# Performance work log

Measured on AMD Instinct MI355X. Metric: run time of the kernel, lower is better.

Reference implementation:

```python
import jax, jax.numpy as jnp
import numpy as np

BN_EPS = 1e-5

def _bn_relu(x, gamma, beta):
    # x: [E, B, F]; BatchNorm1d in training mode: batch stats over B, biased var
    mu = jnp.mean(x, axis=1, keepdims=True)
    var = jnp.mean(jnp.square(x - mu), axis=1, keepdims=True)
    y = gamma[:, None, :] * (x - mu) * jax.lax.rsqrt(var + BN_EPS) + beta[:, None, :]
    return jax.nn.relu(y)

def setup_inputs() -> dict:
    key = jax.random.key(0)
    ks = jax.random.split(key, 4)
    B, D, E, H1, H2, T = 32768, 1472, 8, 512, 256, 2
    s1 = (2.0 / D) ** 0.5
    s2 = (2.0 / H1) ** 0.5
    return {
        "x_deep": jax.random.normal(ks[0], (B, D), jnp.float32),
        "W1": jax.random.normal(ks[1], (E, D, H1), jnp.float32) * s1,
        "b1": jnp.zeros((E, H1), jnp.float32),
        "g1": jnp.ones((E, H1), jnp.float32),
        "be1": jnp.zeros((E, H1), jnp.float32),
        "W2": jax.random.normal(ks[2], (E, H1, H2), jnp.float32) * s2,
        "b2": jnp.zeros((E, H2), jnp.float32),
        "g2": jnp.ones((E, H2), jnp.float32),
        "be2": jnp.zeros((E, H2), jnp.float32),
        "Wg": jax.random.normal(ks[3], (T, D, E), jnp.float32) * s1,
        "bg": jnp.zeros((T, E), jnp.float32),
    }

def reference(x_deep, W1, b1, g1, be1, W2, b2, g2, be2, Wg, bg):
    # Experts: batched over expert dim E (replaces Python loop over nn.ModuleList)
    h = jnp.einsum('bd,edh->ebh', x_deep, W1) + b1[:, None, :]   # [E,B,H1]
    h = _bn_relu(h, g1, be1)                                     # dropout: identity (eval)
    h = jnp.einsum('ebh,ehk->ebk', h, W2) + b2[:, None, :]       # [E,B,H2]
    experts_out = _bn_relu(h, g2, be2)                           # [E,B,H2]
    # Gates: [T,B,E], softmax over experts
    gates = jax.nn.softmax(jnp.einsum('bd,tde->tbe', x_deep, Wg) + bg[:, None, :], axis=-1)
    # Combine: task_out[t] = reshape(experts_out * gate[...,None], [B, E*H2])
    task = experts_out[None, :, :, :] * jnp.transpose(gates, (0, 2, 1))[:, :, :, None]  # [T,E,B,H2]
    T, E, B, H2 = task.shape
    out = jnp.transpose(task, (0, 2, 1, 3)).reshape(T, B, E * H2)  # [T,B,E*H2]
    return out
```

## Files before the change

### kernel.cpp

```cpp
#include <hip/hip_runtime.h>
#include <cstdint>


typedef __attribute__((ext_vector_type(8))) __bf16 bf16x8;
typedef __attribute__((ext_vector_type(4))) float f32x4;

__device__ __forceinline__ unsigned short f2bf(float f) {
  unsigned int u = __float_as_uint(f);
  u += 0x7fffu + ((u >> 16) & 1u);
  return (unsigned short)(u >> 16);
}
__device__ __forceinline__ float bf2f(unsigned short s) {
  return __uint_as_float(((unsigned int)s) << 16);
}

__device__ __forceinline__ void async16(const void* g, void* l) {
  __builtin_amdgcn_global_load_lds((__attribute__((address_space(1))) unsigned int*)g,
                                   (__attribute__((address_space(3))) unsigned int*)l,
                                   16, 0, 0);
}

__global__ void convert_f32_bf16(const float* __restrict__ in,
                                 unsigned short* __restrict__ out, size_t n) {
  size_t i = ((size_t)blockIdx.x * blockDim.x + threadIdx.x) * 4;
  if (i + 3 < n) {
    float4 v = *(const float4*)(in + i);
    unsigned int w0 = (unsigned int)f2bf(v.x) | ((unsigned int)f2bf(v.y) << 16);
    unsigned int w1 = (unsigned int)f2bf(v.z) | ((unsigned int)f2bf(v.w) << 16);
    *(uint2*)(out + i) = make_uint2(w0, w1);
  }
}

__global__ void transpose_bf16(const float* __restrict__ W,
                               unsigned short* __restrict__ Wt, int D, int H) {
  __shared__ float tile[32][33];
  int e = blockIdx.z;
  int d0 = blockIdx.x * 32, h0 = blockIdx.y * 32;
  const float* We = W + (size_t)e * D * H;
  unsigned short* Wte = Wt + (size_t)e * D * H;
  int tx = threadIdx.x, ty = threadIdx.y;
#pragma unroll
  for (int i = 0; i < 4; ++i)
    tile[ty + i * 8][tx] = We[(size_t)(d0 + ty + i * 8) * H + h0 + tx];
  __syncthreads();
#pragma unroll
  for (int i = 0; i < 4; ++i)
    Wte[(size_t)(h0 + ty + i * 8) * D + d0 + tx] = f2bf(tile[tx][ty + i * 8]);
}

__global__ void transpose_wg(const float* __restrict__ Wg,
                             unsigned short* __restrict__ Wt, int D) {
  int idx = blockIdx.x * 256 + threadIdx.x;
  int te = idx / D, d = idx - te * D;
  int t = te >> 3, e = te & 7;
  Wt[(size_t)te * D + d] = f2bf(Wg[((size_t)t * D + d) * 8 + e]);
}

__global__ __launch_bounds__(256) void gemm_bt(
    const unsigned short* __restrict__ A, int lda,
    const unsigned short* __restrict__ Bt,
    unsigned short* __restrict__ C, int ldc, int K,
    size_t aStrideE, size_t bStrideE, size_t cStrideE,
    float* __restrict__ sum, float* __restrict__ sq, int statStrideE, int statCols,
    int groupM, int GN) {
  __shared__ unsigned short sA[128 * 32];
  __shared__ unsigned short sB[128 * 32];
  const int tid = threadIdx.x;
  const int e = blockIdx.z;

  int bx, by;
  if (groupM) {
    int bid = blockIdx.x;
    int gsize = groupM * GN;
    int gid = bid / gsize;
    int rem = bid - gid * gsize;
    bx = gid * groupM + rem % groupM;
    by = rem / groupM;
  } else {
    bx = blockIdx.x; by = blockIdx.y;
  }

  const unsigned short* Ae = A + (size_t)e * aStrideE + (size_t)bx * 128 * lda;
  const unsigned short* Be = Bt + (size_t)e * bStrideE + (size_t)by * 128 * K;

  const int lrow = tid >> 2;
  const int lseg = (tid & 3) * 8;
  const int wid = tid >> 6, lane = tid & 63;
  const int wr = (wid & 1) * 64, wc = (wid >> 1) * 64;
  const int mrow = lane & 15;
  const int kg = (lane >> 4) * 8;

  f32x4 acc[4][4] = {};
  const unsigned short* ga = Ae + (size_t)lrow * lda + lseg;
  const unsigned short* gb = Be + (size_t)lrow * K + lseg;
  const size_t aHalf = (size_t)64 * lda;
  const size_t bHalf = (size_t)64 * K;

  for (int k0 = 0; k0 < K; k0 += 32) {
    async16(ga + k0,         &sA[tid * 8]);
    async16(ga + k0 + aHalf, &sA[2048 + tid * 8]);
    async16(gb + k0,         &sB[tid * 8]);
    async16(gb + k0 + bHalf, &sB[2048 + tid * 8]);
    __syncthreads();
    bf16x8 af[4], bfr[4];
#pragma unroll
    for (int i = 0; i < 4; ++i)
      af[i] = *(const bf16x8*)&sA[(wr + i * 16 + mrow) * 32 + kg];
#pragma unroll
    for (int j = 0; j < 4; ++j)
      bfr[j] = *(const bf16x8*)&sB[(wc + j * 16 + mrow) * 32 + kg];
#pragma unroll
    for (int i = 0; i < 4; ++i)
#pragma unroll
      for (int j = 0; j < 4; ++j)
        acc[i][j] = __builtin_amdgcn_mfma_f32_16x16x32_bf16(af[i], bfr[j], acc[i][j], 0, 0, 0);
    __syncthreads();
  }

  unsigned short* Ce = C + (size_t)e * cStrideE + (size_t)bx * 128 * ldc +
                       (size_t)by * 128;
  const int r0 = wr + (lane >> 4) * 4;
  const int c0 = wc + (lane & 15);
#pragma unroll
  for (int i = 0; i < 4; ++i)
#pragma unroll
    for (int j = 0; j < 4; ++j)
#pragma unroll
      for (int r = 0; r < 4; ++r)
        Ce[(size_t)(r0 + i * 16 + r) * ldc + c0 + j * 16] = f2bf(acc[i][j][r]);

  float* se = sum + (size_t)e * statStrideE;
  float* qe = sq + (size_t)e * statStrideE;
#pragma unroll
  for (int j = 0; j < 4; ++j) {
    float s = 0.f, q = 0.f;
#pragma unroll
    for (int i = 0; i < 4; ++i)
#pragma unroll
      for (int r = 0; r < 4; ++r) {
        float v = acc[i][j][r];
        s += v;
        q = fmaf(v, v, q);
      }
    s += __shfl_xor(s, 16, 64); s += __shfl_xor(s, 32, 64);
    q += __shfl_xor(q, 16, 64); q += __shfl_xor(q, 32, 64);
    if ((lane >> 4) == 0) {
      int col = by * 128 + wc + j * 16 + (lane & 15);
      if (col < statCols) {
        atomicAdd(&se[col], s);
        atomicAdd(&qe[col], q);
      }
    }
  }
}

__global__ void bn_coef(const float* __restrict__ sum, const float* __restrict__ sq,
                        const float* __restrict__ g, const float* __restrict__ be,
                        float* __restrict__ A, float* __restrict__ C, int n, float invB) {
  int i = blockIdx.x * blockDim.x + threadIdx.x;
  if (i < n) {
    float mean = sum[i] * invB;
    float var = sq[i] * invB - mean * mean;
    float a = g[i] * rsqrtf(var + 1e-5f);
    A[i] = a;
    C[i] = be[i] - mean * a;
  }
}

__global__ void gates_softmax(const unsigned short* __restrict__ h1,
                              const float* __restrict__ bg,
                              float* __restrict__ gates, int Bn) {
  int b = blockIdx.x * 256 + threadIdx.x;
  const unsigned short* p = h1 + (size_t)b * 4224 + 4096;
  uint4 v[2];
  v[0] = *(const uint4*)p;
  v[1] = *(const uint4*)(p + 8);
#pragma unroll
  for (int t = 0; t < 2; ++t) {
    float l[8];
    unsigned int w[4] = {v[t].x, v[t].y, v[t].z, v[t].w};
#pragma unroll
    for (int j = 0; j < 4; ++j) {
      l[2 * j]     = __uint_as_float(w[j] << 16) + bg[t * 8 + 2 * j];
      l[2 * j + 1] = __uint_as_float(w[j] & 0xffff0000u) + bg[t * 8 + 2 * j + 1];
    }
    float mx = -1e30f;
#pragma unroll
    for (int e = 0; e < 8; ++e) mx = fmaxf(mx, l[e]);
    float s = 0.f;
#pragma unroll
    for (int e = 0; e < 8; ++e) { l[e] = expf(l[e] - mx); s += l[e]; }
    float inv = 1.f / s;
    float4* gp = (float4*)(gates + ((size_t)t * Bn + b) * 8);
    gp[0] = make_float4(l[0] * inv, l[1] * inv, l[2] * inv, l[3] * inv);
    gp[1] = make_float4(l[4] * inv, l[5] * inv, l[6] * inv, l[7] * inv);
  }
}

__global__ void bn_relu_inplace(unsigned short* __restrict__ h, const float* __restrict__ A,
                                const float* __restrict__ C) {
  int tid = blockIdx.x * blockDim.x + threadIdx.x;
  int r = tid / 528, cb = tid - r * 528;
  if (cb >= 512) return;
  int col = cb * 8;
  size_t i = (size_t)r * 4224 + col;
  uint4 v = *(const uint4*)(h + i);
  unsigned int w[4] = {v.x, v.y, v.z, v.w};
#pragma unroll
  for (int j = 0; j < 4; ++j) {
    float f0 = __uint_as_float(w[j] << 16);
    float f1 = __uint_as_float(w[j] & 0xffff0000u);
    float y0 = fmaxf(fmaf(A[col + 2 * j], f0, C[col + 2 * j]), 0.f);
    float y1 = fmaxf(fmaf(A[col + 2 * j + 1], f1, C[col + 2 * j + 1]), 0.f);
    w[j] = (unsigned int)f2bf(y0) | ((unsigned int)f2bf(y1) << 16);
  }
  *(uint4*)(h + i) = make_uint4(w[0], w[1], w[2], w[3]);
}

__global__ void combine(const unsigned short* __restrict__ h2,
                        const float* __restrict__ A, const float* __restrict__ C,
                        const float* __restrict__ gates,
                        float* __restrict__ out, int Bn) {
  int b = blockIdx.x;
  int c = threadIdx.x * 8;
  int e = c >> 8;
  uint4 v = *(const uint4*)(h2 + (size_t)b * 2048 + c);
  unsigned int w[4] = {v.x, v.y, v.z, v.w};
  float y[8];
#pragma unroll
  for (int j = 0; j < 4; ++j) {
    float f0 = __uint_as_float(w[j] << 16);
    float f1 = __uint_as_float(w[j] & 0xffff0000u);
    y[2 * j]     = fmaxf(fmaf(A[c + 2 * j], f0, C[c + 2 * j]), 0.f);
    y[2 * j + 1] = fmaxf(fmaf(A[c + 2 * j + 1], f1, C[c + 2 * j + 1]), 0.f);
  }
  float g0 = gates[(size_t)b * 8 + e];
  float g1 = gates[((size_t)Bn + b) * 8 + e];
  float4* o0 = (float4*)(out + (size_t)b * 2048 + c);
  float4* o1 = (float4*)(out + ((size_t)Bn + b) * 2048 + c);
  o0[0] = make_float4(y[0] * g0, y[1] * g0, y[2] * g0, y[3] * g0);
  o0[1] = make_float4(y[4] * g0, y[5] * g0, y[6] * g0, y[7] * g0);
  o1[0] = make_float4(y[0] * g1, y[1] * g1, y[2] * g1, y[3] * g1);
  o1[1] = make_float4(y[4] * g1, y[5] * g1, y[6] * g1, y[7] * g1);
}

extern "C" void kernel_launch(void* const* d_in, const int* in_sizes, int n_in,
                              void* d_out, int out_size, void* d_ws, size_t ws_size,
                              hipStream_t stream) {
  const int B = 32768, D = 1472, E = 8, H1 = 512, H2 = 256;
  const int N1 = 4224;
  const float* x   = (const float*)d_in[0];
  const float* W1  = (const float*)d_in[1];
  const float* g1  = (const float*)d_in[3];
  const float* be1 = (const float*)d_in[4];
  const float* W2  = (const float*)d_in[5];
  const float* g2  = (const float*)d_in[7];
  const float* be2 = (const float*)d_in[8];
  const float* Wg  = (const float*)d_in[9];
  const float* bg  = (const float*)d_in[10];
  float* out = (float*)d_out;

  char* p = (char*)d_ws;
  unsigned short* x_b = (unsigned short*)p; p += (size_t)B * D * 2;
  unsigned short* W1t = (unsigned short*)p; p += (size_t)N1 * D * 2;
  unsigned short* W2t = (unsigned short*)p; p += (size_t)E * H2 * H1 * 2;
  unsigned short* h1b = (unsigned short*)p; p += (size_t)B * N1 * 2;
  unsigned short* h2b = (unsigned short*)p; p += (size_t)B * E * H2 * 2;
  float* gatesBuf = (float*)p; p += (size_t)2 * B * 8 * 4;
  float* sum1 = (float*)p; p += (size_t)E * H1 * 4;
  float* sq1  = (float*)p; p += (size_t)E * H1 * 4;
  float* sum2 = (float*)p; p += (size_t)E * H2 * 4;
  float* sq2  = (float*)p; p += (size_t)E * H2 * 4;
  float* A1   = (float*)p; p += (size_t)E * H1 * 4;
  float* C1   = (float*)p; p += (size_t)E * H1 * 4;
  float* A2   = (float*)p; p += (size_t)E * H2 * 4;
  float* C2   = (float*)p; p += (size_t)E * H2 * 4;

  hipMemsetAsync(sum1, 0, (size_t)(2 * E * H1 + 2 * E * H2) * 4, stream);

  convert_f32_bf16<<<(unsigned)((size_t)B * D / (256 * 4)), 256, 0, stream>>>(
      x, x_b, (size_t)B * D);
  transpose_bf16<<<dim3(D / 32, H1 / 32, E), dim3(32, 8), 0, stream>>>(W1, W1t, D, H1);
  transpose_wg<<<(16 * D + 255) / 256, 256, 0, stream>>>(Wg, W1t + (size_t)4096 * D, D);
  transpose_bf16<<<dim3(H1 / 32, H2 / 32, E), dim3(32, 8), 0, stream>>>(W2, W2t, H1, H2);

  gemm_bt<<<dim3(256 * 33), 256, 0, stream>>>(
      x_b, D, W1t, h1b, N1, D, (size_t)0, (size_t)0, (size_t)0,
      sum1, sq1, 0, E * H1, 32, 33);

  bn_coef<<<(E * H1 + 255) / 256, 256, 0, stream>>>(sum1, sq1, g1, be1, A1, C1, E * H1, 1.f / B);
  gates_softmax<<<B / 256, 256, 0, stream>>>(h1b, bg, gatesBuf, B);
  bn_relu_inplace<<<(unsigned)((size_t)B * 528 / 256), 256, 0, stream>>>(h1b, A1, C1);

  gemm_bt<<<dim3(B / 128, H2 / 128, E), 256, 0, stream>>>(
      h1b, N1, W2t, h2b, E * H2, H1,
      (size_t)512, (size_t)H2 * H1, (size_t)256,
      sum2, sq2, H2, H2, 0, 0);

  bn_coef<<<(E * H2 + 255) / 256, 256, 0, stream>>>(sum2, sq2, g2, be2, A2, C2, E * H2, 1.f / B);

  combine<<<B, 256, 0, stream>>>(h2b, A2, C2, gatesBuf, out, B);
}
```

Measured before the change: 1.658 ms.

## Use 256x256 tiled GEMM with 4-stage LDS pipeline and separate MFMA gate kernel

Replaces the 128x128 single-buffered GEMM with a 512-thread 256x256 tile kernel. It uses a 4-deep async global-to-LDS ring with an XOR swizzle, priority boosting around the MFMAs, and an XCD-aware block remap. The gate projection is pulled out of the first GEMM, so N shrinks from 4224 to 4096 and tiles divide evenly, and gates are computed by a small dedicated MFMA kernel with shuffle-based softmax. The larger tiles aim to raise arithmetic intensity and hide load latency, at the cost of 128KB of LDS per block and higher register pressure.

```diff
diff --git a/kernel.cpp b/kernel.cpp
--- a/kernel.cpp
+++ b/kernel.cpp
@@ -9,9 +9,6 @@
   unsigned int u = __float_as_uint(f);
   u += 0x7fffu + ((u >> 16) & 1u);
   return (unsigned short)(u >> 16);
-}
-__device__ __forceinline__ float bf2f(unsigned short s) {
-  return __uint_as_float(((unsigned int)s) << 16);
 }
 
 __device__ __forceinline__ void async16(const void* g, void* l) {
@@ -56,73 +53,99 @@
   Wt[(size_t)te * D + d] = f2bf(Wg[((size_t)t * D + d) * 8 + e]);
 }
 
-__global__ __launch_bounds__(256) void gemm_bt(
+__global__ __launch_bounds__(512, 2) void gemm256(
     const unsigned short* __restrict__ A, int lda,
     const unsigned short* __restrict__ Bt,
     unsigned short* __restrict__ C, int ldc, int K,
     size_t aStrideE, size_t bStrideE, size_t cStrideE,
-    float* __restrict__ sum, float* __restrict__ sq, int statStrideE, int statCols,
-    int groupM, int GN) {
-  __shared__ unsigned short sA[128 * 32];
-  __shared__ unsigned short sB[128 * 32];
+    float* __restrict__ sum, float* __restrict__ sq,
+    int statStrideE, int statCols, int groupM, int GN) {
+  __shared__ __attribute__((aligned(128))) char smem[131072];
   const int tid = threadIdx.x;
+  const int lane = tid & 63;
+  const int wid = tid >> 6;
+  const int wm = wid & 1;
+  const int wn = wid >> 1;
   const int e = blockIdx.z;
 
   int bx, by;
   if (groupM) {
     int bid = blockIdx.x;
+    int cpx = (int)gridDim.x >> 3;
+    int b2 = (bid & 7) * cpx + (bid >> 3);
     int gsize = groupM * GN;
-    int gid = bid / gsize;
-    int rem = bid - gid * gsize;
+    int gid = b2 / gsize;
+    int rem = b2 - gid * gsize;
     bx = gid * groupM + rem % groupM;
     by = rem / groupM;
   } else {
     bx = blockIdx.x; by = blockIdx.y;
   }
 
-  const unsigned short* Ae = A + (size_t)e * aStrideE + (size_t)bx * 128 * lda;
-  const unsigned short* Be = Bt + (size_t)e * bStrideE + (size_t)by * 128 * K;
-
-  const int lrow = tid >> 2;
-  const int lseg = (tid & 3) * 8;
-  const int wid = tid >> 6, lane = tid & 63;
-  const int wr = (wid & 1) * 64, wc = (wid >> 1) * 64;
+  const unsigned short* Ae = A + (size_t)e * aStrideE + (size_t)bx * 256 * lda;
+  const unsigned short* Be = Bt + (size_t)e * bStrideE + (size_t)by * 256 * K;
+
+  const int srow = tid >> 2;
+  const int scol = ((tid & 3) ^ ((tid >> 3) & 3)) * 8;
+  const unsigned short* gA0 = Ae + (size_t)srow * lda + scol;
+  const unsigned short* gA1 = Ae + (size_t)(srow + 128) * lda + scol;
+  const unsigned short* gB0 = Be + (size_t)srow * K + scol;
+  const unsigned short* gB1 = Be + (size_t)(srow + 128) * K + scol;
+  char* ldsStage = smem + tid * 16;
+
   const int mrow = lane & 15;
-  const int kg = (lane >> 4) * 8;
-
-  f32x4 acc[4][4] = {};
-  const unsigned short* ga = Ae + (size_t)lrow * lda + lseg;
-  const unsigned short* gb = Be + (size_t)lrow * K + lseg;
-  const size_t aHalf = (size_t)64 * lda;
-  const size_t bHalf = (size_t)64 * K;
-
-  for (int k0 = 0; k0 < K; k0 += 32) {
-    async16(ga + k0,         &sA[tid * 8]);
-    async16(ga + k0 + aHalf, &sA[2048 + tid * 8]);
-    async16(gb + k0,         &sB[tid * 8]);
-    async16(gb + k0 + bHalf, &sB[2048 + tid * 8]);
-    __syncthreads();
-    bf16x8 af[4], bfr[4];
-#pragma unroll
-    for (int i = 0; i < 4; ++i)
-      af[i] = *(const bf16x8*)&sA[(wr + i * 16 + mrow) * 32 + kg];
-#pragma unroll
-    for (int j = 0; j < 4; ++j)
-      bfr[j] = *(const bf16x8*)&sB[(wc + j * 16 + mrow) * 32 + kg];
-#pragma unroll
-    for (int i = 0; i < 4; ++i)
+  const int cb = (((lane >> 4) ^ ((lane >> 1) & 3)) << 4);
+  const char* rdA = smem + (wm * 128 + mrow) * 64 + cb;
+  const char* rdB = smem + 16384 + (wn * 64 + mrow) * 64 + cb;
+
+  f32x4 acc[8][4] = {};
+  const int NT = K >> 5;
+
+  auto stage = [&](int tt) {
+    char* dst = ldsStage + (tt & 3) * 32768;
+    const int ko = tt * 32;
+    async16(gA0 + ko, dst);
+    async16(gA1 + ko, dst + 8192);
+    async16(gB0 + ko, dst + 16384);
+    async16(gB1 + ko, dst + 24576);
+  };
+  auto compute = [&](int t) {
+    const char* pa = rdA + (t & 3) * 32768;
+    const char* pb = rdB + (t & 3) * 32768;
+    bf16x8 af[8], bfr[4];
+#pragma unroll
+    for (int i = 0; i < 8; ++i) af[i] = *(const bf16x8*)(pa + i * 1024);
+#pragma unroll
+    for (int j = 0; j < 4; ++j) bfr[j] = *(const bf16x8*)(pb + j * 1024);
+    __builtin_amdgcn_s_setprio(1);
+#pragma unroll
+    for (int i = 0; i < 8; ++i)
 #pragma unroll
       for (int j = 0; j < 4; ++j)
         acc[i][j] = __builtin_amdgcn_mfma_f32_16x16x32_bf16(af[i], bfr[j], acc[i][j], 0, 0, 0);
-    __syncthreads();
-  }
-
-  unsigned short* Ce = C + (size_t)e * cStrideE + (size_t)bx * 128 * ldc +
-                       (size_t)by * 128;
-  const int r0 = wr + (lane >> 4) * 4;
-  const int c0 = wc + (lane & 15);
-#pragma unroll
-  for (int i = 0; i < 4; ++i)
+    __builtin_amdgcn_s_setprio(0);
+  };
+
+  stage(0); stage(1);
+  asm volatile("s_waitcnt vmcnt(4)\n\ts_barrier" ::: "memory");
+
+  int t = 0;
+  for (; t < NT - 2; ++t) {
+    stage(t + 2);
+    compute(t);
+    asm volatile("s_waitcnt vmcnt(4)\n\ts_barrier" ::: "memory");
+  }
+  compute(t);
+  asm volatile("s_waitcnt vmcnt(0)\n\ts_barrier" ::: "memory");
+  ++t;
+  compute(t);
+
+  unsigned short* Ce = C + (size_t)e * cStrideE + (size_t)bx * 256 * ldc +
+                       (size_t)by * 256;
+  const int r0 = wm * 128 + (lane >> 4) * 4;
+  const int c0 = wn * 64 + mrow;
+#pragma unroll
+  for (int i = 0; i < 8; ++i)
 #pragma unroll
     for (int j = 0; j < 4; ++j)
 #pragma unroll
@@ -135,7 +158,7 @@
   for (int j = 0; j < 4; ++j) {
     float s = 0.f, q = 0.f;
 #pragma unroll
-    for (int i = 0; i < 4; ++i)
+    for (int i = 0; i < 8; ++i)
 #pragma unroll
       for (int r = 0; r < 4; ++r) {
         float v = acc[i][j][r];
@@ -145,7 +168,7 @@
     s += __shfl_xor(s, 16, 64); s += __shfl_xor(s, 32, 64);
     q += __shfl_xor(q, 16, 64); q += __shfl_xor(q, 32, 64);
     if ((lane >> 4) == 0) {
-      int col = by * 128 + wc + j * 16 + (lane & 15);
+      int col = by * 256 + wn * 64 + j * 16 + mrow;
       if (col < statCols) {
         atomicAdd(&se[col], s);
         atomicAdd(&qe[col], q);
@@ -167,43 +190,51 @@
   }
 }
 
-__global__ void gates_softmax(const unsigned short* __restrict__ h1,
-                              const float* __restrict__ bg,
-                              float* __restrict__ gates, int Bn) {
-  int b = blockIdx.x * 256 + threadIdx.x;
-  const unsigned short* p = h1 + (size_t)b * 4224 + 4096;
-  uint4 v[2];
-  v[0] = *(const uint4*)p;
-  v[1] = *(const uint4*)(p + 8);
-#pragma unroll
-  for (int t = 0; t < 2; ++t) {
-    float l[8];
-    unsigned int w[4] = {v[t].x, v[t].y, v[t].z, v[t].w};
-#pragma unroll
-    for (int j = 0; j < 4; ++j) {
-      l[2 * j]     = __uint_as_float(w[j] << 16) + bg[t * 8 + 2 * j];
-      l[2 * j + 1] = __uint_as_float(w[j] & 0xffff0000u) + bg[t * 8 + 2 * j + 1];
-    }
-    float mx = -1e30f;
-#pragma unroll
-    for (int e = 0; e < 8; ++e) mx = fmaxf(mx, l[e]);
-    float s = 0.f;
-#pragma unroll
-    for (int e = 0; e < 8; ++e) { l[e] = expf(l[e] - mx); s += l[e]; }
-    float inv = 1.f / s;
-    float4* gp = (float4*)(gates + ((size_t)t * Bn + b) * 8);
-    gp[0] = make_float4(l[0] * inv, l[1] * inv, l[2] * inv, l[3] * inv);
-    gp[1] = make_float4(l[4] * inv, l[5] * inv, l[6] * inv, l[7] * inv);
+__global__ __launch_bounds__(256) void gates_mfma(
+    const unsigned short* __restrict__ xb,
+    const unsigned short* __restrict__ wgt,
+    const float* __restrict__ bg,
+    float* __restrict__ gates, int Bn) {
+  const int lane = threadIdx.x & 63;
+  const int w = threadIdx.x >> 6;
+  const int row0 = blockIdx.x * 64 + w * 16;
+  const int mrow = lane & 15, kseg = (lane >> 4) * 8;
+  const unsigned short* pa = xb + (size_t)(row0 + mrow) * 1472 + kseg;
+  const unsigned short* pb = wgt + (size_t)mrow * 1472 + kseg;
+  f32x4 acc = {};
+  bf16x8 a0 = *(const bf16x8*)pa, b0 = *(const bf16x8*)pb;
+  for (int ks = 1; ks < 46; ++ks) {
+    bf16x8 a1 = *(const bf16x8*)(pa + ks * 32);
+    bf16x8 b1 = *(const bf16x8*)(pb + ks * 32);
+    acc = __builtin_amdgcn_mfma_f32_16x16x32_bf16(a0, b0, acc, 0, 0, 0);
+    a0 = a1; b0 = b1;
+  }
+  acc = __builtin_amdgcn_mfma_f32_16x16x32_bf16(a0, b0, acc, 0, 0, 0);
+  const int c = lane & 15;
+  const float bias = bg[c];
+#pragma unroll
+  for (int r = 0; r < 4; ++r) {
+    float v = acc[r] + bias;
+    float m = v;
+    m = fmaxf(m, __shfl_xor(m, 1, 64));
+    m = fmaxf(m, __shfl_xor(m, 2, 64));
+    m = fmaxf(m, __shfl_xor(m, 4, 64));
+    float p = expf(v - m);
+    float s = p;
+    s += __shfl_xor(s, 1, 64);
+    s += __shfl_xor(s, 2, 64);
+    s += __shfl_xor(s, 4, 64);
+    int rowg = row0 + (lane >> 4) * 4 + r;
+    gates[((size_t)(c >> 3) * Bn + rowg) * 8 + (c & 7)] = p / s;
   }
 }
 
 __global__ void bn_relu_inplace(unsigned short* __restrict__ h, const float* __restrict__ A,
                                 const float* __restrict__ C) {
   int tid = blockIdx.x * blockDim.x + threadIdx.x;
-  int r = tid / 528, cb = tid - r * 528;
-  if (cb >= 512) return;
+  int r = tid >> 9, cb = tid & 511;
   int col = cb * 8;
-  size_t i = (size_t)r * 4224 + col;
+  size_t i = (size_t)r * 4096 + col;
   uint4 v = *(const uint4*)(h + i);
   unsigned int w[4] = {v.x, v.y, v.z, v.w};
 #pragma unroll
@@ -248,7 +279,7 @@
                               void* d_out, int out_size, void* d_ws, size_t ws_size,
                               hipStream_t stream) {
   const int B = 32768, D = 1472, E = 8, H1 = 512, H2 = 256;
-  const int N1 = 4224;
+  const int N1 = E * H1;
   const float* x   = (const float*)d_in[0];
   const float* W1  = (const float*)d_in[1];
   const float* g1  = (const float*)d_in[3];
@@ -263,41 +294,42 @@
   char* p = (char*)d_ws;
   unsigned short* x_b = (unsigned short*)p; p += (size_t)B * D * 2;
   unsigned short* W1t = (unsigned short*)p; p += (size_t)N1 * D * 2;
+  unsigned short* Wgt = (unsigned short*)p; p += (size_t)16 * D * 2;
   unsigned short* W2t = (unsigned short*)p; p += (size_t)E * H2 * H1 * 2;
   unsigned short* h1b = (unsigned short*)p; p += (size_t)B * N1 * 2;
   unsigned short* h2b = (unsigned short*)p; p += (size_t)B * E * H2 * 2;
   float* gatesBuf = (float*)p; p += (size_t)2 * B * 8 * 4;
-  float* sum1 = (float*)p; p += (size_t)E * H1 * 4;
-  float* sq1  = (float*)p; p += (size_t)E * H1 * 4;
+  float* sum1 = (float*)p; p += (size_t)N1 * 4;
+  float* sq1  = (float*)p; p += (size_t)N1 * 4;
   float* sum2 = (float*)p; p += (size_t)E * H2 * 4;
   float* sq2  = (float*)p; p += (size_t)E * H2 * 4;
-  float* A1   = (float*)p; p += (size_t)E * H1 * 4;
-  float* C1   = (float*)p; p += (size_t)E * H1 * 4;
+  float* A1   = (float*)p; p += (size_t)N1 * 4;
+  float* C1   = (float*)p; p += (size_t)N1 * 4;
   float* A2   = (float*)p; p += (size_t)E * H2 * 4;
   float* C2   = (float*)p; p += (size_t)E * H2 * 4;
 
-  hipMemsetAsync(sum1, 0, (size_t)(2 * E * H1 + 2 * E * H2) * 4, stream);
-
-  convert_f32_bf16<<<(unsigned)((size_t)B * D / (256 * 4)), 256, 0, stream>>>(
+  hipMemsetAsync(sum1, 0, (size_t)(2 * N1 + 2 * E * H2) * 4, stream);
+
+  convert_f32_bf16<<<(unsigned)((size_t)B * D / 1024), 256, 0, stream>>>(
       x, x_b, (size_t)B * D);
   transpose_bf16<<<dim3(D / 32, H1 / 32, E), dim3(32, 8), 0, stream>>>(W1, W1t, D, H1);
-  transpose_wg<<<(16 * D + 255) / 256, 256, 0, stream>>>(Wg, W1t + (size_t)4096 * D, D);
+  transpose_wg<<<16 * D / 256, 256, 0, stream>>>(Wg, Wgt, D);
   transpose_bf16<<<dim3(H1 / 32, H2 / 32, E), dim3(32, 8), 0, stream>>>(W2, W2t, H1, H2);
 
-  gemm_bt<<<dim3(256 * 33), 256, 0, stream>>>(
+  gemm256<<<dim3(128 * 16), 512, 0, stream>>>(
       x_b, D, W1t, h1b, N1, D, (size_t)0, (size_t)0, (size_t)0,
-      sum1, sq1, 0, E * H1, 32, 33);
-
-  bn_coef<<<(E * H1 + 255) / 256, 256, 0, stream>>>(sum1, sq1, g1, be1, A1, C1, E * H1, 1.f / B);
-  gates_softmax<<<B / 256, 256, 0, stream>>>(h1b, bg, gatesBuf, B);
-  bn_relu_inplace<<<(unsigned)((size_t)B * 528 / 256), 256, 0, stream>>>(h1b, A1, C1);
-
-  gemm_bt<<<dim3(B / 128, H2 / 128, E), 256, 0, stream>>>(
+      sum1, sq1, 0, N1, 16, 16);
+
+  bn_coef<<<N1 / 256, 256, 0, stream>>>(sum1, sq1, g1, be1, A1, C1, N1, 1.f / B);
+  gates_mfma<<<B / 64, 256, 0, stream>>>(x_b, Wgt, bg, gatesBuf, B);
+  bn_relu_inplace<<<(unsigned)((size_t)B * 512 / 256), 256, 0, stream>>>(h1b, A1, C1);
+
+  gemm256<<<dim3(B / 256, 1, E), 512, 0, stream>>>(
       h1b, N1, W2t, h2b, E * H2, H1,
-      (size_t)512, (size_t)H2 * H1, (size_t)256,
+      (size_t)H1, (size_t)H1 * H2, (size_t)H2,
       sum2, sq2, H2, H2, 0, 0);
 
-  bn_coef<<<(E * H2 + 255) / 256, 256, 0, stream>>>(sum2, sq2, g2, be2, A2, C2, E * H2, 1.f / B);
+  bn_coef<<<E * H2 / 256, 256, 0, stream>>>(sum2, sq2, g2, be2, A2, C2, E * H2, 1.f / B);
 
   combine<<<B, 256, 0, stream>>>(h2b, A2, C2, gatesBuf, out, B);
 }
```

Measured after the change: 1.454 ms. 12.3% less time.
